# Kernel tuning notes

Measured on AMD Instinct MI355X. Metric: run time of the kernel, lower is better.

The kernel has to match this reference:

```python
import jax, jax.numpy as jnp
import numpy as np

N_NODES = 40000


def gcn_conv(x, W, b, src, dst, deg_inv_sqrt, n_nodes):
    # x: [N, Din], W: [Din, Dout]
    h = x @ W  # [N, Dout]
    norm = deg_inv_sqrt[src] * deg_inv_sqrt[dst]  # [E'] (edges incl. self-loops)
    msg = h[src] * norm[:, None]  # gather + scale: [E', Dout]
    out = jax.ops.segment_sum(msg, dst, num_segments=n_nodes)  # scatter-add
    return out + b


def setup_inputs() -> dict:
    key = jax.random.key(0)
    k1, k2, k3, k4, k5, k6 = jax.random.split(key, 6)
    x = jax.random.normal(k1, (N_NODES, 512), dtype=jnp.float32)
    edge_index = jax.random.randint(k2, (2, 640000), 0, N_NODES, dtype=jnp.int64)
    W1 = jax.random.normal(k3, (512, 256), dtype=jnp.float32) * (1.0 / np.sqrt(512))
    b1 = jax.random.normal(k4, (256,), dtype=jnp.float32) * 0.01
    W2 = jax.random.normal(k5, (256, 47), dtype=jnp.float32) * (1.0 / np.sqrt(256))
    b2 = jax.random.normal(k6, (47,), dtype=jnp.float32) * 0.01
    return {"x": x, "edge_index": edge_index, "W1": W1, "b1": b1, "W2": W2, "b2": b2}


def reference(x, edge_index, W1, b1, W2, b2):
    n = x.shape[0]
    loops = jnp.arange(n, dtype=edge_index.dtype)
    # add self-loops (PyG GCNConv default)
    src = jnp.concatenate([edge_index[0], loops])
    dst = jnp.concatenate([edge_index[1], loops])
    # symmetric normalization: deg over A + I (unit edge weights)
    deg = jax.ops.segment_sum(jnp.ones_like(dst, dtype=x.dtype), dst, num_segments=n)
    deg_inv_sqrt = jnp.where(deg > 0, jax.lax.rsqrt(jnp.maximum(deg, 1e-12)), 0.0)

    h = gcn_conv(x, W1, b1, src, dst, deg_inv_sqrt, n)
    h = jax.nn.relu(h)
    # dropout is identity in eval mode (training=False)
    h = gcn_conv(h, W2, b2, src, dst, deg_inv_sqrt, n)
    return jax.nn.log_softmax(h, axis=1)
```

## Files before the change

### kernel.cpp

```cpp
#include <hip/hip_runtime.h>


typedef _Float16 f16;
typedef _Float16 f16x8 __attribute__((ext_vector_type(8)));
typedef _Float16 f16x4 __attribute__((ext_vector_type(4)));
typedef float f32x4 __attribute__((ext_vector_type(4)));

#define N_NODES 40000
#define N_EDGES 640000
#define D_IN 512
#define D_HID 256
#define D_OUT 47
#define D_OUT_PAD 48


__global__ void k_degree(const int* __restrict__ eidx, int* __restrict__ deg) {
    int e = blockIdx.x * blockDim.x + threadIdx.x;
    if (e < N_EDGES) atomicAdd(&deg[eidx[N_EDGES + e]], 1);
}

__global__ __launch_bounds__(1024) void k_scan(const int* __restrict__ deg,
                                               int* __restrict__ rowptr,
                                               float* __restrict__ dinv) {
    __shared__ int wsum[16];
    const int S = 40;
    int t = threadIdx.x;
    int lane = t & 63;
    int wid = t >> 6;
    int base = t * S;
    bool live = (base < N_NODES);

    int v[S];
    int tot = 0;
#pragma unroll
    for (int i = 0; i < S / 4; ++i) {
        int4 q = make_int4(0, 0, 0, 0);
        if (live) q = *(const int4*)(deg + base + i * 4);
        v[i * 4 + 0] = q.x; v[i * 4 + 1] = q.y;
        v[i * 4 + 2] = q.z; v[i * 4 + 3] = q.w;
        tot += q.x + q.y + q.z + q.w;
    }
    int inc = tot;
#pragma unroll
    for (int off = 1; off < 64; off <<= 1) {
        int n = __shfl_up(inc, off);
        if (lane >= off) inc += n;
    }
    if (lane == 63) wsum[wid] = inc;
    __syncthreads();
    if (t < 16) {
        int wv = wsum[t];
        int winc = wv;
#pragma unroll
        for (int off = 1; off < 16; off <<= 1) {
            int n = __shfl_up(winc, off);
            if (t >= off) winc += n;
        }
        wsum[t] = winc - wv;
    }
    __syncthreads();
    int acc = wsum[wid] + (inc - tot);
#pragma unroll
    for (int i = 0; i < S / 4; ++i) {
        int4 r; float4 f;
        r.x = acc; f.x = rsqrtf((float)(v[i * 4 + 0] + 1)); acc += v[i * 4 + 0];
        r.y = acc; f.y = rsqrtf((float)(v[i * 4 + 1] + 1)); acc += v[i * 4 + 1];
        r.z = acc; f.z = rsqrtf((float)(v[i * 4 + 2] + 1)); acc += v[i * 4 + 2];
        r.w = acc; f.w = rsqrtf((float)(v[i * 4 + 3] + 1)); acc += v[i * 4 + 3];
        if (live) {
            *(int4*)(rowptr + base + i * 4) = r;
            *(float4*)(dinv + base + i * 4) = f;
        }
    }
    if (t == 0) rowptr[N_NODES] = N_EDGES;
}

__global__ void k_fill(const int* __restrict__ eidx, const int* __restrict__ rowptr,
                       int* __restrict__ cursor, int* __restrict__ col) {
    int e = blockIdx.x * blockDim.x + threadIdx.x;
    if (e < N_EDGES) {
        int s = eidx[e];
        int d = eidx[N_EDGES + e];
        int pos = atomicAdd(&cursor[d], 1);
        col[rowptr[d] + pos] = s;
    }
}


__global__ void k_pack_w1(const float* __restrict__ W, f16* __restrict__ Wp) {
    int u = blockIdx.x * blockDim.x + threadIdx.x;
    if (u >= 16 * 16 * 64) return;
    int l = u & 63;
    int nf = (u >> 6) & 15;
    int kt = u >> 10;
    int k0 = kt * 32 + (l >> 4) * 8;
    int c = nf * 16 + (l & 15);
    f16x8 o;
#pragma unroll
    for (int j = 0; j < 8; ++j) o[j] = (f16)W[(size_t)(k0 + j) * D_HID + c];
    *(f16x8*)(Wp + (size_t)u * 8) = o;
}

__global__ void k_pack_w2(const float* __restrict__ W, f16* __restrict__ Wp) {
    int u = blockIdx.x * blockDim.x + threadIdx.x;
    if (u >= 8 * 3 * 64) return;
    int l = u & 63;
    int nf = (u / 64) % 3;
    int kt = u / 192;
    int k0 = kt * 32 + (l >> 4) * 8;
    int c = nf * 16 + (l & 15);
    f16x8 o;
#pragma unroll
    for (int j = 0; j < 8; ++j)
        o[j] = (c < D_OUT) ? (f16)W[(size_t)(k0 + j) * D_OUT + c] : (f16)0.0f;
    *(f16x8*)(Wp + (size_t)u * 8) = o;
}


__global__ __launch_bounds__(512) void k_gemm1(const float* __restrict__ X,
                                               const f16* __restrict__ Bp,
                                               f16* __restrict__ C) {
    __shared__ f16 As[64][520];
    int t = threadIdx.x;
    int lane = t & 63;
    int wid = t >> 6;
    int rowBase = blockIdx.x * 64;

#pragma unroll
    for (int it = 0; it < 16; ++it) {
        int idx = it * 512 + t;
        int row = idx >> 7;
        int c4 = idx & 127;
        float4 v = *(const float4*)(X + (size_t)(rowBase + row) * D_IN + c4 * 4);
        f16x4 o;
        o[0] = (f16)v.x; o[1] = (f16)v.y; o[2] = (f16)v.z; o[3] = (f16)v.w;
        *(f16x4*)(&As[row][c4 * 4]) = o;
    }
    __syncthreads();

    int nf0 = wid * 2;
    int r_ = lane & 15, q_ = lane >> 4;

    f32x4 acc[4][2];
#pragma unroll
    for (int mi = 0; mi < 4; ++mi)
#pragma unroll
        for (int ni = 0; ni < 2; ++ni) acc[mi][ni] = (f32x4)(0.0f);

#pragma unroll 4
    for (int kt = 0; kt < 16; ++kt) {
        f16x8 a[4], b[2];
#pragma unroll
        for (int mi = 0; mi < 4; ++mi)
            a[mi] = *(const f16x8*)(&As[mi * 16 + r_][kt * 32 + q_ * 8]);
#pragma unroll
        for (int ni = 0; ni < 2; ++ni)
            b[ni] = *(const f16x8*)(Bp + ((size_t)(kt * 16 + nf0 + ni) * 64 + lane) * 8);
#pragma unroll
        for (int mi = 0; mi < 4; ++mi)
#pragma unroll
            for (int ni = 0; ni < 2; ++ni)
                acc[mi][ni] = __builtin_amdgcn_mfma_f32_16x16x32_f16(a[mi], b[ni], acc[mi][ni], 0, 0, 0);
    }

    int r0 = q_ * 4;
    int c0 = r_;
#pragma unroll
    for (int mi = 0; mi < 4; ++mi)
#pragma unroll
        for (int ni = 0; ni < 2; ++ni)
#pragma unroll
            for (int r = 0; r < 4; ++r) {
                int row = rowBase + mi * 16 + r0 + r;
                C[(size_t)row * D_HID + (nf0 + ni) * 16 + c0] = (f16)acc[mi][ni][r];
            }
}


__global__ __launch_bounds__(256) void k_gemm2(const f16* __restrict__ Ap,
                                               const f16* __restrict__ Bp,
                                               f16* __restrict__ C) {
    int wid = threadIdx.x >> 6;
    int lane = threadIdx.x & 63;
    int rowTile = blockIdx.x * 4 + wid;
    int rowBase = rowTile * 64;
    if (rowBase >= N_NODES) return;

    f32x4 acc[4][3];
#pragma unroll
    for (int mi = 0; mi < 4; ++mi)
#pragma unroll
        for (int ni = 0; ni < 3; ++ni) acc[mi][ni] = (f32x4)(0.0f);

    int m16b = rowTile * 4;
    for (int kt = 0; kt < 8; ++kt) {
        f16x8 a[4], b[3];
#pragma unroll
        for (int mi = 0; mi < 4; ++mi)
            a[mi] = *(const f16x8*)(Ap + ((size_t)((m16b + mi) * 8 + kt) * 64 + lane) * 8);
#pragma unroll
        for (int ni = 0; ni < 3; ++ni)
            b[ni] = *(const f16x8*)(Bp + ((size_t)(kt * 3 + ni) * 64 + lane) * 8);
#pragma unroll
        for (int mi = 0; mi < 4; ++mi)
#pragma unroll
            for (int ni = 0; ni < 3; ++ni)
                acc[mi][ni] = __builtin_amdgcn_mfma_f32_16x16x32_f16(a[mi], b[ni], acc[mi][ni], 0, 0, 0);
    }

    int r0 = (lane >> 4) * 4;
    int c0 = lane & 15;
#pragma unroll
    for (int mi = 0; mi < 4; ++mi)
#pragma unroll
        for (int ni = 0; ni < 3; ++ni)
#pragma unroll
            for (int r = 0; r < 4; ++r) {
                int row = rowBase + mi * 16 + r0 + r;
                C[(size_t)row * D_OUT_PAD + ni * 16 + c0] = (f16)acc[mi][ni][r];
            }
}


__global__ __launch_bounds__(256) void k_agg1(const f16* __restrict__ h1,
                                              const int* __restrict__ rowptr,
                                              const int* __restrict__ col,
                                              const float* __restrict__ dinv,
                                              const float* __restrict__ b1,
                                              f16* __restrict__ hp) {
    int node = blockIdx.x * 4 + (threadIdx.x >> 6);
    int lane = threadIdx.x & 63;
    int half = lane >> 5;
    int hl = lane & 31;
    float di = dinv[node];

    f16x8 selfv = *(const f16x8*)(h1 + (size_t)node * D_HID + hl * 8);

    float a[8];
#pragma unroll
    for (int j = 0; j < 8; ++j) a[j] = 0.0f;

    int e0 = rowptr[node], e1 = rowptr[node + 1];
    for (int base = e0; base < e1; base += 64) {
        int nn = min(64, e1 - base);
        int sidx = 0; float wv = 0.0f;
        if (lane < nn) {
            int s = col[base + lane];
            sidx = s;
            wv = dinv[s] * di;
        }
        int t = half;
        for (; t + 6 < nn; t += 8) {
            int s0 = __shfl(sidx, t),     s1 = __shfl(sidx, t + 2);
            int s2 = __shfl(sidx, t + 4), s3 = __shfl(sidx, t + 6);
            float w0 = __shfl(wv, t),     w1 = __shfl(wv, t + 2);
            float w2 = __shfl(wv, t + 4), w3 = __shfl(wv, t + 6);
            f16x8 u0 = *(const f16x8*)(h1 + (size_t)s0 * D_HID + hl * 8);
            f16x8 u1 = *(const f16x8*)(h1 + (size_t)s1 * D_HID + hl * 8);
            f16x8 u2 = *(const f16x8*)(h1 + (size_t)s2 * D_HID + hl * 8);
            f16x8 u3 = *(const f16x8*)(h1 + (size_t)s3 * D_HID + hl * 8);
#pragma unroll
            for (int j = 0; j < 8; ++j)
                a[j] += (float)u0[j] * w0 + (float)u1[j] * w1 +
                        (float)u2[j] * w2 + (float)u3[j] * w3;
        }
        for (; t + 2 < nn; t += 4) {
            int s0 = __shfl(sidx, t), s1 = __shfl(sidx, t + 2);
            float w0 = __shfl(wv, t), w1 = __shfl(wv, t + 2);
            f16x8 u0 = *(const f16x8*)(h1 + (size_t)s0 * D_HID + hl * 8);
            f16x8 u1 = *(const f16x8*)(h1 + (size_t)s1 * D_HID + hl * 8);
#pragma unroll
            for (int j = 0; j < 8; ++j)
                a[j] += (float)u0[j] * w0 + (float)u1[j] * w1;
        }
        if (t < nn) {
            int s0 = __shfl(sidx, t);
            float w0 = __shfl(wv, t);
            f16x8 u0 = *(const f16x8*)(h1 + (size_t)s0 * D_HID + hl * 8);
#pragma unroll
            for (int j = 0; j < 8; ++j) a[j] += (float)u0[j] * w0;
        }
    }

#pragma unroll
    for (int j = 0; j < 8; ++j) a[j] += __shfl_xor(a[j], 32);

    float wself = di * di;
    float4 b_lo = *(const float4*)(b1 + hl * 8);
    float4 b_hi = *(const float4*)(b1 + hl * 8 + 4);
    f16x8 o;
    o[0] = (f16)fmaxf(a[0] + (float)selfv[0] * wself + b_lo.x, 0.0f);
    o[1] = (f16)fmaxf(a[1] + (float)selfv[1] * wself + b_lo.y, 0.0f);
    o[2] = (f16)fmaxf(a[2] + (float)selfv[2] * wself + b_lo.z, 0.0f);
    o[3] = (f16)fmaxf(a[3] + (float)selfv[3] * wself + b_lo.w, 0.0f);
    o[4] = (f16)fmaxf(a[4] + (float)selfv[4] * wself + b_hi.x, 0.0f);
    o[5] = (f16)fmaxf(a[5] + (float)selfv[5] * wself + b_hi.y, 0.0f);
    o[6] = (f16)fmaxf(a[6] + (float)selfv[6] * wself + b_hi.z, 0.0f);
    o[7] = (f16)fmaxf(a[7] + (float)selfv[7] * wself + b_hi.w, 0.0f);

    if (half == 0) {
        size_t idx = ((size_t)(node >> 4) * 8 + (hl >> 2)) * 512 + (hl & 3) * 128 + (node & 15) * 8;
        *(f16x8*)(hp + idx) = o;
    }
}


__global__ __launch_bounds__(256) void k_agg2(const f16* __restrict__ g,
                                              const int* __restrict__ rowptr,
                                              const int* __restrict__ col,
                                              const float* __restrict__ dinv,
                                              const float* __restrict__ b2,
                                              float* __restrict__ out) {
    int node = blockIdx.x * 4 + (threadIdx.x >> 6);
    int lane = threadIdx.x & 63;
    float di = dinv[node];
    bool act = lane < D_OUT_PAD;
    float acc = act ? (float)g[(size_t)node * D_OUT_PAD + lane] * di * di : 0.0f;

    int e0 = rowptr[node], e1 = rowptr[node + 1];
    for (int base = e0; base < e1; base += 64) {
        int nn = min(64, e1 - base);
        int sidx = 0; float wv = 0.0f;
        if (lane < nn) {
            int s = col[base + lane];
            sidx = s;
            wv = dinv[s] * di;
        }
        int k = 0;
        for (; k + 8 <= nn; k += 8) {
            int s0 = __shfl(sidx, k),     s1 = __shfl(sidx, k + 1);
            int s2 = __shfl(sidx, k + 2), s3 = __shfl(sidx, k + 3);
            int s4 = __shfl(sidx, k + 4), s5 = __shfl(sidx, k + 5);
            int s6 = __shfl(sidx, k + 6), s7 = __shfl(sidx, k + 7);
            float w0 = __shfl(wv, k),     w1 = __shfl(wv, k + 1);
            float w2 = __shfl(wv, k + 2), w3 = __shfl(wv, k + 3);
            float w4 = __shfl(wv, k + 4), w5 = __shfl(wv, k + 5);
            float w6 = __shfl(wv, k + 6), w7 = __shfl(wv, k + 7);
            if (act) {
                float u0 = (float)g[(size_t)s0 * D_OUT_PAD + lane];
                float u1 = (float)g[(size_t)s1 * D_OUT_PAD + lane];
                float u2 = (float)g[(size_t)s2 * D_OUT_PAD + lane];
                float u3 = (float)g[(size_t)s3 * D_OUT_PAD + lane];
                float u4 = (float)g[(size_t)s4 * D_OUT_PAD + lane];
                float u5 = (float)g[(size_t)s5 * D_OUT_PAD + lane];
                float u6 = (float)g[(size_t)s6 * D_OUT_PAD + lane];
                float u7 = (float)g[(size_t)s7 * D_OUT_PAD + lane];
                acc += u0 * w0 + u1 * w1 + u2 * w2 + u3 * w3 +
                       u4 * w4 + u5 * w5 + u6 * w6 + u7 * w7;
            }
        }
        for (; k < nn; ++k) {
            int s0 = __shfl(sidx, k);
            float w0 = __shfl(wv, k);
            if (act) acc += (float)g[(size_t)s0 * D_OUT_PAD + lane] * w0;
        }
    }

    float z = (lane < D_OUT) ? acc + b2[lane] : -3.0e38f;
    float mx = z;
#pragma unroll
    for (int off = 32; off >= 1; off >>= 1) mx = fmaxf(mx, __shfl_xor(mx, off));
    float ex = (lane < D_OUT) ? expf(z - mx) : 0.0f;
    float sum = ex;
#pragma unroll
    for (int off = 32; off >= 1; off >>= 1) sum += __shfl_xor(sum, off);
    if (lane < D_OUT) out[(size_t)node * D_OUT + lane] = z - mx - logf(sum);
}


extern "C" void kernel_launch(void* const* d_in, const int* in_sizes, int n_in,
                              void* d_out, int out_size, void* d_ws, size_t ws_size,
                              hipStream_t stream) {
    const float* x  = (const float*)d_in[0];
    const int*   ei = (const int*)d_in[1];
    const float* W1 = (const float*)d_in[2];
    const float* b1 = (const float*)d_in[3];
    const float* W2 = (const float*)d_in[4];
    const float* b2 = (const float*)d_in[5];
    float* out = (float*)d_out;

    char* ws = (char*)d_ws;
    int*   degi   = (int*)(ws + 0);
    int*   cursor = (int*)(ws + 160000);
    float* dinv   = (float*)(ws + 320000);
    int*   rowptr = (int*)(ws + 480000);
    int*   col    = (int*)(ws + 640256);
    f16*   w1p    = (f16*)(ws + 3200256);
    f16*   w2p    = (f16*)(ws + 3462400);
    f16*   h1     = (f16*)(ws + 3486976);
    f16*   hpk    = (f16*)(ws + 23966976);
    f16*   g      = (f16*)(ws + 44446976);

    hipMemsetAsync(d_ws, 0, 320000, stream);

    k_degree<<<2500, 256, 0, stream>>>(ei, degi);
    k_scan<<<1, 1024, 0, stream>>>(degi, rowptr, dinv);
    k_fill<<<2500, 256, 0, stream>>>(ei, rowptr, cursor, col);

    k_pack_w1<<<64, 256, 0, stream>>>(W1, w1p);
    k_pack_w2<<<6, 256, 0, stream>>>(W2, w2p);

    k_gemm1<<<625, 512, 0, stream>>>(x, w1p, h1);
    k_agg1<<<10000, 256, 0, stream>>>(h1, rowptr, col, dinv, b1, hpk);
    k_gemm2<<<157, 256, 0, stream>>>(hpk, w2p, g);
    k_agg2<<<10000, 256, 0, stream>>>(g, rowptr, col, dinv, b2, out);
}
```

Baseline: 199.4 us.

## Fuse layer-1 aggregation with layer-2 GEMM via shared memory; merge init kernels

Layer-1 aggregation and the layer-2 GEMM now run in one kernel. Each block aggregates 64 nodes (16 per wave) into a shared-memory tile, then three waves run MFMA against packed W2 to write g directly. This removes the packed hpk intermediate and its global round-trip, and one launch. The weight packing and the workspace zeroing are also folded into a single init kernel that replaces the memset and two launches. In exchange the aggregation grid drops from 10000 blocks of one node per wave to 625 blocks, with each wave serially processing 16 nodes. That cuts parallelism and latency hiding for the gather-bound step, and one wave sits idle during the GEMM.

New measurement: 193.9 us. -2.7%, faster.

```diff
diff --git a/kernel.cpp b/kernel.cpp
--- a/kernel.cpp
+++ b/kernel.cpp
@@ -12,6 +12,42 @@
 #define D_HID 256
 #define D_OUT 47
 #define D_OUT_PAD 48
+#define HS_LD 262
+
+
+__global__ void k_init(const float* __restrict__ W1, const float* __restrict__ W2,
+                       f16* __restrict__ w1p, f16* __restrict__ w2p,
+                       int* __restrict__ zeroes) {
+    int bid = blockIdx.x;
+    int t = threadIdx.x;
+    if (bid < 64) {
+        int u = bid * 256 + t;
+        int l = u & 63;
+        int nf = (u >> 6) & 15;
+        int kt = u >> 10;
+        int k0 = kt * 32 + (l >> 4) * 8;
+        int c = nf * 16 + (l & 15);
+        f16x8 o;
+#pragma unroll
+        for (int j = 0; j < 8; ++j) o[j] = (f16)W1[(size_t)(k0 + j) * D_HID + c];
+        *(f16x8*)(w1p + (size_t)u * 8) = o;
+    } else if (bid < 70) {
+        int u = (bid - 64) * 256 + t;
+        int l = u & 63;
+        int nf = (u / 64) % 3;
+        int kt = u / 192;
+        int k0 = kt * 32 + (l >> 4) * 8;
+        int c = nf * 16 + (l & 15);
+        f16x8 o;
+#pragma unroll
+        for (int j = 0; j < 8; ++j)
+            o[j] = (c < D_OUT) ? (f16)W2[(size_t)(k0 + j) * D_OUT + c] : (f16)0.0f;
+        *(f16x8*)(w2p + (size_t)u * 8) = o;
+    } else {
+        int i = (bid - 70) * 256 + t;
+        if (i < 80000) zeroes[i] = 0;
+    }
+}
 
 
 __global__ void k_degree(const int* __restrict__ eidx, int* __restrict__ deg) {
@@ -87,36 +123,6 @@
 }
 
 
-__global__ void k_pack_w1(const float* __restrict__ W, f16* __restrict__ Wp) {
-    int u = blockIdx.x * blockDim.x + threadIdx.x;
-    if (u >= 16 * 16 * 64) return;
-    int l = u & 63;
-    int nf = (u >> 6) & 15;
-    int kt = u >> 10;
-    int k0 = kt * 32 + (l >> 4) * 8;
-    int c = nf * 16 + (l & 15);
-    f16x8 o;
-#pragma unroll
-    for (int j = 0; j < 8; ++j) o[j] = (f16)W[(size_t)(k0 + j) * D_HID + c];
-    *(f16x8*)(Wp + (size_t)u * 8) = o;
-}
-
-__global__ void k_pack_w2(const float* __restrict__ W, f16* __restrict__ Wp) {
-    int u = blockIdx.x * blockDim.x + threadIdx.x;
-    if (u >= 8 * 3 * 64) return;
-    int l = u & 63;
-    int nf = (u / 64) % 3;
-    int kt = u / 192;
-    int k0 = kt * 32 + (l >> 4) * 8;
-    int c = nf * 16 + (l & 15);
-    f16x8 o;
-#pragma unroll
-    for (int j = 0; j < 8; ++j)
-        o[j] = (c < D_OUT) ? (f16)W[(size_t)(k0 + j) * D_OUT + c] : (f16)0.0f;
-    *(f16x8*)(Wp + (size_t)u * 8) = o;
-}
-
-
 __global__ __launch_bounds__(512) void k_gemm1(const float* __restrict__ X,
                                                const f16* __restrict__ Bp,
                                                f16* __restrict__ C) {
@@ -177,130 +183,118 @@
 }
 
 
-__global__ __launch_bounds__(256) void k_gemm2(const f16* __restrict__ Ap,
-                                               const f16* __restrict__ Bp,
-                                               f16* __restrict__ C) {
-    int wid = threadIdx.x >> 6;
-    int lane = threadIdx.x & 63;
-    int rowTile = blockIdx.x * 4 + wid;
-    int rowBase = rowTile * 64;
-    if (rowBase >= N_NODES) return;
-
-    f32x4 acc[4][3];
-#pragma unroll
-    for (int mi = 0; mi < 4; ++mi)
-#pragma unroll
-        for (int ni = 0; ni < 3; ++ni) acc[mi][ni] = (f32x4)(0.0f);
-
-    int m16b = rowTile * 4;
-    for (int kt = 0; kt < 8; ++kt) {
-        f16x8 a[4], b[3];
-#pragma unroll
-        for (int mi = 0; mi < 4; ++mi)
-            a[mi] = *(const f16x8*)(Ap + ((size_t)((m16b + mi) * 8 + kt) * 64 + lane) * 8);
-#pragma unroll
-        for (int ni = 0; ni < 3; ++ni)
-            b[ni] = *(const f16x8*)(Bp + ((size_t)(kt * 3 + ni) * 64 + lane) * 8);
-#pragma unroll
-        for (int mi = 0; mi < 4; ++mi)
-#pragma unroll
-            for (int ni = 0; ni < 3; ++ni)
-                acc[mi][ni] = __builtin_amdgcn_mfma_f32_16x16x32_f16(a[mi], b[ni], acc[mi][ni], 0, 0, 0);
-    }
-
-    int r0 = (lane >> 4) * 4;
-    int c0 = lane & 15;
-#pragma unroll
-    for (int mi = 0; mi < 4; ++mi)
-#pragma unroll
-        for (int ni = 0; ni < 3; ++ni)
-#pragma unroll
-            for (int r = 0; r < 4; ++r) {
-                int row = rowBase + mi * 16 + r0 + r;
-                C[(size_t)row * D_OUT_PAD + ni * 16 + c0] = (f16)acc[mi][ni][r];
-            }
-}
-
-
-__global__ __launch_bounds__(256) void k_agg1(const f16* __restrict__ h1,
-                                              const int* __restrict__ rowptr,
-                                              const int* __restrict__ col,
-                                              const float* __restrict__ dinv,
-                                              const float* __restrict__ b1,
-                                              f16* __restrict__ hp) {
-    int node = blockIdx.x * 4 + (threadIdx.x >> 6);
-    int lane = threadIdx.x & 63;
+__global__ __launch_bounds__(256) void k_agg1g2(const f16* __restrict__ h1,
+                                                const int* __restrict__ rowptr,
+                                                const int* __restrict__ col,
+                                                const float* __restrict__ dinv,
+                                                const float* __restrict__ b1,
+                                                const f16* __restrict__ w2p,
+                                                f16* __restrict__ g) {
+    __shared__ f16 hs[64][HS_LD];
+    int t = threadIdx.x;
+    int lane = t & 63;
+    int wid = t >> 6;
     int half = lane >> 5;
     int hl = lane & 31;
-    float di = dinv[node];
-
-    f16x8 selfv = *(const f16x8*)(h1 + (size_t)node * D_HID + hl * 8);
-
-    float a[8];
-#pragma unroll
-    for (int j = 0; j < 8; ++j) a[j] = 0.0f;
-
-    int e0 = rowptr[node], e1 = rowptr[node + 1];
-    for (int base = e0; base < e1; base += 64) {
-        int nn = min(64, e1 - base);
-        int sidx = 0; float wv = 0.0f;
-        if (lane < nn) {
-            int s = col[base + lane];
-            sidx = s;
-            wv = dinv[s] * di;
-        }
-        int t = half;
-        for (; t + 6 < nn; t += 8) {
-            int s0 = __shfl(sidx, t),     s1 = __shfl(sidx, t + 2);
-            int s2 = __shfl(sidx, t + 4), s3 = __shfl(sidx, t + 6);
-            float w0 = __shfl(wv, t),     w1 = __shfl(wv, t + 2);
-            float w2 = __shfl(wv, t + 4), w3 = __shfl(wv, t + 6);
-            f16x8 u0 = *(const f16x8*)(h1 + (size_t)s0 * D_HID + hl * 8);
-            f16x8 u1 = *(const f16x8*)(h1 + (size_t)s1 * D_HID + hl * 8);
-            f16x8 u2 = *(const f16x8*)(h1 + (size_t)s2 * D_HID + hl * 8);
-            f16x8 u3 = *(const f16x8*)(h1 + (size_t)s3 * D_HID + hl * 8);
-#pragma unroll
-            for (int j = 0; j < 8; ++j)
-                a[j] += (float)u0[j] * w0 + (float)u1[j] * w1 +
-                        (float)u2[j] * w2 + (float)u3[j] * w3;
-        }
-        for (; t + 2 < nn; t += 4) {
-            int s0 = __shfl(sidx, t), s1 = __shfl(sidx, t + 2);
-            float w0 = __shfl(wv, t), w1 = __shfl(wv, t + 2);
-            f16x8 u0 = *(const f16x8*)(h1 + (size_t)s0 * D_HID + hl * 8);
-            f16x8 u1 = *(const f16x8*)(h1 + (size_t)s1 * D_HID + hl * 8);
-#pragma unroll
-            for (int j = 0; j < 8; ++j)
-                a[j] += (float)u0[j] * w0 + (float)u1[j] * w1;
-        }
-        if (t < nn) {
-            int s0 = __shfl(sidx, t);
-            float w0 = __shfl(wv, t);
-            f16x8 u0 = *(const f16x8*)(h1 + (size_t)s0 * D_HID + hl * 8);
-#pragma unroll
-            for (int j = 0; j < 8; ++j) a[j] += (float)u0[j] * w0;
-        }
-    }
-
-#pragma unroll
-    for (int j = 0; j < 8; ++j) a[j] += __shfl_xor(a[j], 32);
-
-    float wself = di * di;
+    int nodeBase = blockIdx.x * 64 + wid * 16;
+
     float4 b_lo = *(const float4*)(b1 + hl * 8);
     float4 b_hi = *(const float4*)(b1 + hl * 8 + 4);
-    f16x8 o;
-    o[0] = (f16)fmaxf(a[0] + (float)selfv[0] * wself + b_lo.x, 0.0f);
-    o[1] = (f16)fmaxf(a[1] + (float)selfv[1] * wself + b_lo.y, 0.0f);
-    o[2] = (f16)fmaxf(a[2] + (float)selfv[2] * wself + b_lo.z, 0.0f);
-    o[3] = (f16)fmaxf(a[3] + (float)selfv[3] * wself + b_lo.w, 0.0f);
-    o[4] = (f16)fmaxf(a[4] + (float)selfv[4] * wself + b_hi.x, 0.0f);
-    o[5] = (f16)fmaxf(a[5] + (float)selfv[5] * wself + b_hi.y, 0.0f);
-    o[6] = (f16)fmaxf(a[6] + (float)selfv[6] * wself + b_hi.z, 0.0f);
-    o[7] = (f16)fmaxf(a[7] + (float)selfv[7] * wself + b_hi.w, 0.0f);
-
-    if (half == 0) {
-        size_t idx = ((size_t)(node >> 4) * 8 + (hl >> 2)) * 512 + (hl & 3) * 128 + (node & 15) * 8;
-        *(f16x8*)(hp + idx) = o;
+
+    for (int i = 0; i < 16; ++i) {
+        int node = nodeBase + i;
+        float di = dinv[node];
+        f16x8 selfv = *(const f16x8*)(h1 + (size_t)node * D_HID + hl * 8);
+
+        float a[8];
+#pragma unroll
+        for (int j = 0; j < 8; ++j) a[j] = 0.0f;
+
+        int e0 = rowptr[node], e1 = rowptr[node + 1];
+        for (int base = e0; base < e1; base += 64) {
+            int nn = min(64, e1 - base);
+            int sidx = 0; float wv = 0.0f;
+            if (lane < nn) {
+                int s = col[base + lane];
+                sidx = s;
+                wv = dinv[s] * di;
+            }
+            int e = half;
+            for (; e + 6 < nn; e += 8) {
+                int s0 = __shfl(sidx, e),     s1 = __shfl(sidx, e + 2);
+                int s2 = __shfl(sidx, e + 4), s3 = __shfl(sidx, e + 6);
+                float w0 = __shfl(wv, e),     w1 = __shfl(wv, e + 2);
+                float w2 = __shfl(wv, e + 4), w3 = __shfl(wv, e + 6);
+                f16x8 u0 = *(const f16x8*)(h1 + (size_t)s0 * D_HID + hl * 8);
+                f16x8 u1 = *(const f16x8*)(h1 + (size_t)s1 * D_HID + hl * 8);
+                f16x8 u2 = *(const f16x8*)(h1 + (size_t)s2 * D_HID + hl * 8);
+                f16x8 u3 = *(const f16x8*)(h1 + (size_t)s3 * D_HID + hl * 8);
+#pragma unroll
+                for (int j = 0; j < 8; ++j)
+                    a[j] += (float)u0[j] * w0 + (float)u1[j] * w1 +
+                            (float)u2[j] * w2 + (float)u3[j] * w3;
+            }
+            for (; e + 2 < nn; e += 4) {
+                int s0 = __shfl(sidx, e), s1 = __shfl(sidx, e + 2);
+                float w0 = __shfl(wv, e), w1 = __shfl(wv, e + 2);
+                f16x8 u0 = *(const f16x8*)(h1 + (size_t)s0 * D_HID + hl * 8);
+                f16x8 u1 = *(const f16x8*)(h1 + (size_t)s1 * D_HID + hl * 8);
+#pragma unroll
+                for (int j = 0; j < 8; ++j)
+                    a[j] += (float)u0[j] * w0 + (float)u1[j] * w1;
+            }
+            if (e < nn) {
+                int s0 = __shfl(sidx, e);
+                float w0 = __shfl(wv, e);
+                f16x8 u0 = *(const f16x8*)(h1 + (size_t)s0 * D_HID + hl * 8);
+#pragma unroll
+                for (int j = 0; j < 8; ++j) a[j] += (float)u0[j] * w0;
+            }
+        }
+
+#pragma unroll
+        for (int j = 0; j < 8; ++j) a[j] += __shfl_xor(a[j], 32);
+
+        float wself = di * di;
+        f16x8 o;
+        o[0] = (f16)fmaxf(a[0] + (float)selfv[0] * wself + b_lo.x, 0.0f);
+        o[1] = (f16)fmaxf(a[1] + (float)selfv[1] * wself + b_lo.y, 0.0f);
+        o[2] = (f16)fmaxf(a[2] + (float)selfv[2] * wself + b_lo.z, 0.0f);
+        o[3] = (f16)fmaxf(a[3] + (float)selfv[3] * wself + b_lo.w, 0.0f);
+        o[4] = (f16)fmaxf(a[4] + (float)selfv[4] * wself + b_hi.x, 0.0f);
+        o[5] = (f16)fmaxf(a[5] + (float)selfv[5] * wself + b_hi.y, 0.0f);
+        o[6] = (f16)fmaxf(a[6] + (float)selfv[6] * wself + b_hi.z, 0.0f);
+        o[7] = (f16)fmaxf(a[7] + (float)selfv[7] * wself + b_hi.w, 0.0f);
+
+        if (half == 0) *(f16x8*)(&hs[wid * 16 + i][hl * 8]) = o;
+    }
+    __syncthreads();
+
+    if (wid < 3) {
+        int nf = wid;
+        int r_ = lane & 15, q_ = lane >> 4;
+        f32x4 acc[4];
+#pragma unroll
+        for (int mi = 0; mi < 4; ++mi) acc[mi] = (f32x4)(0.0f);
+
+#pragma unroll
+        for (int kt = 0; kt < 8; ++kt) {
+            f16x8 b = *(const f16x8*)(w2p + ((size_t)(kt * 3 + nf) * 64 + lane) * 8);
+#pragma unroll
+            for (int mi = 0; mi < 4; ++mi) {
+                f16x8 a = *(const f16x8*)(&hs[mi * 16 + r_][kt * 32 + q_ * 8]);
+                acc[mi] = __builtin_amdgcn_mfma_f32_16x16x32_f16(a, b, acc[mi], 0, 0, 0);
+            }
+        }
+
+        int rowBase = blockIdx.x * 64;
+#pragma unroll
+        for (int mi = 0; mi < 4; ++mi)
+#pragma unroll
+            for (int r = 0; r < 4; ++r) {
+                int row = rowBase + mi * 16 + q_ * 4 + r;
+                g[(size_t)row * D_OUT_PAD + nf * 16 + r_] = (f16)acc[mi][r];
+            }
     }
 }
 
@@ -388,20 +382,14 @@
     f16*   w1p    = (f16*)(ws + 3200256);
     f16*   w2p    = (f16*)(ws + 3462400);
     f16*   h1     = (f16*)(ws + 3486976);
-    f16*   hpk    = (f16*)(ws + 23966976);
-    f16*   g      = (f16*)(ws + 44446976);
-
-    hipMemsetAsync(d_ws, 0, 320000, stream);
-
+    f16*   g      = (f16*)(ws + 23966976);
+
+    k_init<<<383, 256, 0, stream>>>(W1, W2, w1p, w2p, degi);
     k_degree<<<2500, 256, 0, stream>>>(ei, degi);
     k_scan<<<1, 1024, 0, stream>>>(degi, rowptr, dinv);
     k_fill<<<2500, 256, 0, stream>>>(ei, rowptr, cursor, col);
 
-    k_pack_w1<<<64, 256, 0, stream>>>(W1, w1p);
-    k_pack_w2<<<6, 256, 0, stream>>>(W2, w2p);
-
     k_gemm1<<<625, 512, 0, stream>>>(x, w1p, h1);
-    k_agg1<<<10000, 256, 0, stream>>>(h1, rowptr, col, dinv, b1, hpk);
-    k_gemm2<<<157, 256, 0, stream>>>(hpk, w2p, g);
+    k_agg1g2<<<625, 256, 0, stream>>>(h1, rowptr, col, dinv, b1, w2p, g);
     k_agg2<<<10000, 256, 0, stream>>>(g, rowptr, col, dinv, b2, out);
 }
```
